# Optimization experiments

Measured on AMD Instinct MI355X. Metric: run time of the kernel, lower is better.

The kernel has to match this reference:

```python
import jax, jax.numpy as jnp
import numpy as np

E = 256   # embed_dim
L = 64    # num_landmarks
C = 256   # in_channels
N_ITER = 6


def iterative_inv(K):
    # Newton-Schulz pseudo-inverse on small [*, L, L] matrices (faithful to torch code)
    I = jnp.eye(K.shape[-1], dtype=K.dtype)
    KA = jnp.abs(K)
    V0 = KA.sum(axis=-2, keepdims=True).max(axis=-1, keepdims=True)  # [*,1,1]
    VI = KA.sum(axis=-1, keepdims=True).max(axis=-2, keepdims=True)  # [*,1,1]
    V = jnp.swapaxes(K, -1, -2) / (V0 * VI)
    for _ in range(N_ITER):
        KV = K @ V
        V = 0.25 * V @ (13.0 * I - KV @ (15.0 * I - KV @ (7.0 * I - KV)))
    return V


def setup_inputs() -> dict:
    key = jax.random.key(0)
    k0, k1, k2 = jax.random.split(key, 3)
    x = jax.random.normal(k0, (8, C, 64, 64), dtype=jnp.float32)
    # Conv2d 1x1 weights stored as [out, in]
    w_qkv = jax.random.normal(k1, (3 * E, C), dtype=jnp.float32) * 0.02
    b_qkv = jnp.zeros((3 * E,), dtype=jnp.float32)
    w_out = jax.random.normal(k2, (C, E), dtype=jnp.float32) * 0.02
    b_out = jnp.zeros((C,), dtype=jnp.float32)
    return {"x": x, "w_qkv": w_qkv, "b_qkv": b_qkv, "w_out": w_out, "b_out": b_out}


def reference(x, w_qkv, b_qkv, w_out, b_out):
    N, Cin, H, W = x.shape
    HW = H * W
    # 1x1 conv: [N, 3E, H, W]
    y = jnp.einsum('nchw,ec->nehw', x, w_qkv) + b_qkv[None, :, None, None]
    # faithful raw reshape (mixes channel/spatial like the torch code)
    qkv = y.reshape(N, HW, 3 * E)
    q, k, v = jnp.split(qkv, 3, axis=-1)                     # each [N, HW, E]
    scale = HW ** 0.5
    q_land = q.reshape(N, L, HW // L, E).mean(axis=-2) / scale  # [N, L, E]
    k_land = k.reshape(N, L, HW // L, E).mean(axis=-2) / scale  # [N, L, E]
    # three softmaxes, all over dim=-2 as in the original
    k1 = jax.nn.softmax(jnp.einsum('nie,nje->nij', q, k_land), axis=-2)       # [N, HW, L]
    k2 = jax.nn.softmax(jnp.einsum('nie,nje->nij', q_land, k_land), axis=-2)  # [N, L, L]
    k3 = jax.nn.softmax(jnp.einsum('nie,nje->nij', q_land, k), axis=-2)       # [N, L, HW]
    k2_inv = iterative_inv(k2)
    out = k1 @ (k2_inv @ (k3 @ v)) + v                        # [N, HW, E]
    out = out.reshape(N, E, H, W)                             # faithful raw reshape
    return jnp.einsum('nehw,ce->nchw', out, w_out) + b_out[None, :, None, None]
```

## Files before the change

kernel.cpp:

```cpp
#include <hip/hip_runtime.h>
#include <hip/hip_bf16.h>

typedef unsigned short u16;
typedef __attribute__((ext_vector_type(4))) float f32x4;
typedef __attribute__((ext_vector_type(8))) short short8;

#define NB   8
#define CIN  256
#define EDIM 256
#define M3   768
#define HWN  4096
#define LND  64
#define NS2  72

__device__ __forceinline__ float bf2f(u16 u){ return __uint_as_float(((unsigned)u)<<16); }
__device__ __forceinline__ u16 f2bf(float f){ __hip_bfloat16 h = __float2bfloat16(f); return *reinterpret_cast<u16*>(&h); }
__device__ __forceinline__ void bf2x2(unsigned u, float &lo, float &hi){
  lo = __uint_as_float(u<<16);
  hi = __uint_as_float(u & 0xffff0000u);
}

typedef __attribute__((address_space(1))) unsigned as1_uint;
typedef __attribute__((address_space(3))) unsigned as3_uint;
__device__ __forceinline__ void gl16(const void* g, void* l){
  __builtin_amdgcn_global_load_lds((const as1_uint*)g, (as3_uint*)l, 16, 0, 0);
}

__global__ __launch_bounds__(256) void k_prep(const float* __restrict__ x, u16* __restrict__ Xt,
                                              const float* __restrict__ wq, const float* __restrict__ wo,
                                              u16* __restrict__ Wqb, u16* __restrict__ Wob){
  const int bi = blockIdx.x;
  const int tid = threadIdx.x;
  if(bi >= 2048){
    int ti = (bi-2048)*256 + tid;
    const float* src; u16* dst;
    if(ti < 1536){ src = wq + (size_t)ti*128;        dst = Wqb + (size_t)ti*128; }
    else         { src = wo + (size_t)(ti-1536)*128; dst = Wob + (size_t)(ti-1536)*128; }
    #pragma unroll
    for(int t=0;t<128;t+=8){
      float4 v0 = *(const float4*)(src+t);
      float4 v1 = *(const float4*)(src+t+4);
      ushort4 o0, o1;
      o0.x=f2bf(v0.x); o0.y=f2bf(v0.y); o0.z=f2bf(v0.z); o0.w=f2bf(v0.w);
      o1.x=f2bf(v1.x); o1.y=f2bf(v1.y); o1.z=f2bf(v1.z); o1.w=f2bf(v1.w);
      *(ushort4*)(dst+t)   = o0;
      *(ushort4*)(dst+t+4) = o1;
    }
    return;
  }
  __shared__ float Ts[64*65];
  const int n = bi>>8, rem = bi&255, ct = rem>>6, pt = rem&63;
  const int c0 = ct*64, p0 = pt*64;
  {
    int cc = tid>>2, pj = (tid&3)*16;
    const float* xp = x + (size_t)n*CIN*HWN + (size_t)(c0+cc)*HWN + p0 + pj;
    #pragma unroll
    for(int j=0;j<16;j++) Ts[cc*65 + pj + j] = xp[j];
  }
  __syncthreads();
  {
    int pp = tid>>2, ej = (tid&3)*16;
    u16* op = Xt + ((size_t)n*HWN + p0 + pp)*CIN + c0 + ej;
    ushort4 o[4];
    #pragma unroll
    for(int j=0;j<16;j++) ((u16*)o)[j] = f2bf(Ts[(ej+j)*65 + pp]);
    *(ushort4*)(op+0)  = o[0];
    *(ushort4*)(op+4)  = o[1];
    *(ushort4*)(op+8)  = o[2];
    *(ushort4*)(op+12) = o[3];
  }
}

__global__ __launch_bounds__(256) void k_qkv(const u16* __restrict__ Wb, const u16* __restrict__ Xt,
                                             const float* __restrict__ bias, u16* __restrict__ Y){
  __shared__ __align__(16) u16 As[128*64];
  __shared__ __align__(16) u16 Bs[128*64];
  const int bi = blockIdx.x;
  const int n = bi&7, rem = bi>>3;
  const int ch0 = (rem%6)*128, p0 = (rem/6)*128;
  const int tid = threadIdx.x, lane = tid&63;
  const int c = tid&15, qq = (tid>>4)&3, w4 = tid>>6;
  const int wr0 = (w4&1)*64, wc0 = (w4>>1)*64;
  const u16* xb = Xt + ((size_t)n*HWN + p0)*CIN;
  const u16* wb = Wb + (size_t)ch0*CIN;
  f32x4 acc[4][4];
  #pragma unroll
  for(int mt=0;mt<4;mt++)
    #pragma unroll
    for(int nt=0;nt<4;nt++){ acc[mt][nt][0]=0.f; acc[mt][nt][1]=0.f; acc[mt][nt][2]=0.f; acc[mt][nt][3]=0.f; }
  const int srow  = w4*8 + (lane>>3);
  const int dslot = lane&7;
  const int sgo   = (dslot ^ (lane>>3))*8;
  const int rdswz = (c&7);
  for(int ph=0; ph<4; ph++){
    #pragma unroll
    for(int j=0;j<4;j++){
      int r = j*32 + srow;
      gl16(wb + (size_t)r*CIN + ph*64 + sgo, &As[r*64 + dslot*8]);
    }
    #pragma unroll
    for(int j=0;j<4;j++){
      int r = j*32 + srow;
      gl16(xb + (size_t)r*CIN + ph*64 + sgo, &Bs[r*64 + dslot*8]);
    }
    __syncthreads();
    #pragma unroll
    for(int kt=0;kt<2;kt++){
      short8 af[4], bff[4];
      const int rslot = ((kt*4+qq)^rdswz)*8;
      #pragma unroll
      for(int mt=0;mt<4;mt++) af[mt]  = *(const short8*)&As[(wr0+mt*16+c)*64 + rslot];
      #pragma unroll
      for(int nt=0;nt<4;nt++) bff[nt] = *(const short8*)&Bs[(wc0+nt*16+c)*64 + rslot];
      #pragma unroll
      for(int mt=0;mt<4;mt++)
        #pragma unroll
        for(int nt=0;nt<4;nt++)
          acc[mt][nt] = __builtin_amdgcn_mfma_f32_16x16x32_bf16(af[mt], bff[nt], acc[mt][nt], 0, 0, 0);
    }
    __syncthreads();
  }
  u16* Yb = Y + (size_t)n*M3*HWN;
  #pragma unroll
  for(int mt=0;mt<4;mt++){
    int chb = ch0 + wr0 + mt*16 + 4*qq;
    float b0 = bias[chb], b1 = bias[chb+1], b2 = bias[chb+2], b3 = bias[chb+3];
    #pragma unroll
    for(int nt=0;nt<4;nt++){
      int p = p0 + wc0 + nt*16 + c;
      u16* yp = Yb + (size_t)chb*HWN + p;
      yp[0]             = f2bf(acc[mt][nt][0]+b0);
      yp[HWN]           = f2bf(acc[mt][nt][1]+b1);
      yp[2*(size_t)HWN] = f2bf(acc[mt][nt][2]+b2);
      yp[3*(size_t)HWN] = f2bf(acc[mt][nt][3]+b3);
    }
  }
}

__global__ void k_land(const u16* __restrict__ Y, float* __restrict__ qland, float* __restrict__ kland){
  const int l = blockIdx.x, n = blockIdx.y, e = threadIdx.x;
  const u16* base = Y + (size_t)n*M3*HWN;
  float qs=0.f, ks=0.f;
  #pragma unroll 8
  for(int m=0;m<64;m++){
    size_t off = (size_t)(l*64+m)*M3;
    qs += bf2f(base[off+e]);
    ks += bf2f(base[off+256+e]);
  }
  qland[((size_t)n*LND+l)*EDIM+e] = qs*(1.f/4096.f);
  kland[((size_t)n*LND+l)*EDIM+e] = ks*(1.f/4096.f);
}

__device__ __forceinline__ void ns_mm2(const u16* L, int sL, const u16* Rt, int sR,
                                       int wv, int q, int c, f32x4 r4[4]){
  short8 a0 = *(const short8*)(L + (size_t)(16*wv + c)*sL + 8*q);
  short8 a1 = *(const short8*)(L + (size_t)(16*wv + c)*sL + 32 + 8*q);
  #pragma unroll
  for(int tc=0;tc<4;tc++){
    f32x4 acc = {0.f,0.f,0.f,0.f};
    short8 b0 = *(const short8*)(Rt + (size_t)(16*tc + c)*sR + 8*q);
    short8 b1 = *(const short8*)(Rt + (size_t)(16*tc + c)*sR + 32 + 8*q);
    acc = __builtin_amdgcn_mfma_f32_16x16x32_bf16(a0, b0, acc, 0, 0, 0);
    acc = __builtin_amdgcn_mfma_f32_16x16x32_bf16(a1, b1, acc, 0, 0, 0);
    r4[tc] = acc;
  }
}

#define TTS 64
__device__ void ns_body(int n, char* smem, const float* __restrict__ qland,
                        const float* __restrict__ kland, float* __restrict__ KinvT){
  u16* Kb  = (u16*)(smem + 0);
  u16* Vb  = (u16*)(smem + 9216);
  u16* Vt  = (u16*)(smem + 18432);
  u16* KVb = (u16*)(smem + 27648);
  u16* KVt = (u16*)(smem + 36864);
  u16* Tt  = (u16*)(smem + 46080);
  float* sS   = (float*)(smem + 27648);
  float* sred = (float*)(smem + 44544);
  const int tid = threadIdx.x;
  const int wv = tid>>6, q = (tid>>4)&3, c = tid&15;
  const float* qb = qland + (size_t)n*LND*EDIM;
  const float* kb = kland + (size_t)n*LND*EDIM;
  f32x4 acc[4];
  #pragma unroll
  for(int t=0;t<4;t++){ acc[t][0]=0.f; acc[t][1]=0.f; acc[t][2]=0.f; acc[t][3]=0.f; }
  for(int e0=0;e0<EDIM;e0+=64){
    __syncthreads();
    {
      int row = tid>>2, c0 = (tid&3)*16;
      const float* qp = qb + (size_t)row*EDIM + e0 + c0;
      const float* kp = kb + (size_t)row*EDIM + e0 + c0;
      u16* qd = &KVb[row*NS2 + c0];
      u16* kd = &KVt[row*NS2 + c0];
      #pragma unroll
      for(int j=0;j<16;j+=4){
        float4 qv = *(const float4*)(qp+j);
        float4 kv = *(const float4*)(kp+j);
        ushort4 qo, ko;
        qo.x=f2bf(qv.x); qo.y=f2bf(qv.y); qo.z=f2bf(qv.z); qo.w=f2bf(qv.w);
        ko.x=f2bf(kv.x); ko.y=f2bf(kv.y); ko.z=f2bf(kv.z); ko.w=f2bf(kv.w);
        *(ushort4*)(qd+j) = qo;
        *(ushort4*)(kd+j) = ko;
      }
    }
    __syncthreads();
    {
      short8 a0 = *(const short8*)&KVb[(16*wv+c)*NS2 + 8*q];
      short8 a1 = *(const short8*)&KVb[(16*wv+c)*NS2 + 32 + 8*q];
      #pragma unroll
      for(int tc=0;tc<4;tc++){
        short8 b0 = *(const short8*)&KVt[(16*tc+c)*NS2 + 8*q];
        short8 b1 = *(const short8*)&KVt[(16*tc+c)*NS2 + 32 + 8*q];
        acc[tc] = __builtin_amdgcn_mfma_f32_16x16x32_bf16(a0, b0, acc[tc], 0, 0, 0);
        acc[tc] = __builtin_amdgcn_mfma_f32_16x16x32_bf16(a1, b1, acc[tc], 0, 0, 0);
      }
    }
  }
  __syncthreads();
  #pragma unroll
  for(int tc=0;tc<4;tc++){
    int col = 16*tc + c, row0 = 16*wv + 4*q;
    sS[(row0+0)*66+col] = acc[tc][0];
    sS[(row0+1)*66+col] = acc[tc][1];
    sS[(row0+2)*66+col] = acc[tc][2];
    sS[(row0+3)*66+col] = acc[tc][3];
  }
  __syncthreads();
  if(tid < 64){
    int j = tid;
    float m = -1e30f;
    for(int i=0;i<64;i++) m = fmaxf(m, sS[i*66+j]);
    float ssum = 0.f;
    for(int i=0;i<64;i++) ssum += __expf(sS[i*66+j]-m);
    float inv = 1.f/ssum, cs = 0.f;
    for(int i=0;i<64;i++){
      float kv = __expf(sS[i*66+j]-m)*inv;
      cs += fabsf(kv);
      Kb[i*NS2+j] = f2bf(kv);
    }
    sred[j] = cs;
  }
  __syncthreads();
  if(tid < 64){
    int i = tid; float rs = 0.f;
    for(int j=0;j<64;j++) rs += fabsf(bf2f(Kb[i*NS2+j]));
    sred[64+i] = rs;
  }
  __syncthreads();
  if(tid == 0){
    float v0=-1e30f, vi=-1e30f;
    for(int t=0;t<64;t++){ v0 = fmaxf(v0, sred[t]); vi = fmaxf(vi, sred[64+t]); }
    sred[128] = 1.f/(v0*vi);
  }
  __syncthreads();
  {
    float sc = sred[128];
    int i = tid>>2, j16 = (tid&3)*16;
    #pragma unroll
    for(int jj=0;jj<16;jj++){
      int j = j16+jj;
      u16 bvv = f2bf(bf2f(Kb[j*NS2+i])*sc);
      Vb[i*NS2+j] = bvv;
      Vt[j*NS2+i] = bvv;
    }
  }
  __syncthreads();
  f32x4 r4[4];
  for(int it=0; it<6; it++){
    ns_mm2(Kb, NS2, Vt, NS2, wv, q, c, r4);
    #pragma unroll
    for(int tc=0;tc<4;tc++){
      int col = 16*tc + c, row0 = 16*wv + 4*q;
      ushort4 pk;
      pk.x = f2bf(r4[tc][0]); pk.y = f2bf(r4[tc][1]); pk.z = f2bf(r4[tc][2]); pk.w = f2bf(r4[tc][3]);
      KVb[(row0+0)*NS2+col] = pk.x; KVb[(row0+1)*NS2+col] = pk.y;
      KVb[(row0+2)*NS2+col] = pk.z; KVb[(row0+3)*NS2+col] = pk.w;
      *(ushort4*)&KVt[(size_t)col*NS2 + row0] = pk;
    }
    __syncthreads();
    ns_mm2(KVb, NS2, KVt, NS2, wv, q, c, r4);
    #pragma unroll
    for(int tc=0;tc<4;tc++){
      int col = 16*tc+c, row0 = 16*wv+4*q;
      ushort4 pk;
      #pragma unroll
      for(int r=0;r<4;r++){
        float kvv = bf2f(KVb[(row0+r)*NS2+col]);
        ((u16*)&pk)[r] = f2bf(7.f*kvv - r4[tc][r]);
      }
      *(ushort4*)&Tt[(size_t)col*TTS + row0] = pk;
    }
    __syncthreads();
    ns_mm2(KVb, NS2, Tt, TTS, wv, q, c, r4);
    __syncthreads();
    #pragma unroll
    for(int tc=0;tc<4;tc++){
      int col = 16*tc+c, row0 = 16*wv+4*q;
      ushort4 pk;
      #pragma unroll
      for(int r=0;r<4;r++){
        float kvv = bf2f(KVb[(row0+r)*NS2+col]);
        ((u16*)&pk)[r] = f2bf(15.f*kvv - r4[tc][r]);
      }
      *(ushort4*)&Tt[(size_t)col*TTS + row0] = pk;
    }
    __syncthreads();
    ns_mm2(Vb, NS2, Tt, TTS, wv, q, c, r4);
    __syncthreads();
    #pragma unroll
    for(int tc=0;tc<4;tc++){
      int col = 16*tc+c, row0 = 16*wv+4*q;
      float nv[4]; ushort4 pk;
      #pragma unroll
      for(int r=0;r<4;r++){
        float vv = bf2f(Vb[(row0+r)*NS2+col]);
        nv[r] = 0.25f*(13.f*vv - r4[tc][r]);
        u16 bb = f2bf(nv[r]);
        Vb[(row0+r)*NS2+col] = bb;
        ((u16*)&pk)[r] = bb;
      }
      *(ushort4*)&Vt[(size_t)col*NS2 + row0] = pk;
      if(it==5){
        *(float4*)&KinvT[(size_t)n*4096 + (size_t)col*64 + row0] = make_float4(nv[0],nv[1],nv[2],nv[3]);
      }
    }
    __syncthreads();
  }
}

#define LGS 264
__global__ __launch_bounds__(256) void k_landgemm(const u16* __restrict__ Y, const float* __restrict__ qland,
                                                  const float* __restrict__ kland, float* __restrict__ Z1,
                                                  float* __restrict__ Z3, float* __restrict__ KinvT){
  __shared__ __align__(16) char usm[54272];
  const int z = blockIdx.y;
  if(blockIdx.x == 64){
    if((z&1)==0) ns_body(z>>1, usm, qland, kland, KinvT);
    return;
  }
  u16* As = (u16*)usm;
  u16* BsU = (u16*)(usm + 33792);
  const int n = z>>1, which = z&1;
  const int b0 = blockIdx.x*64;
  const float* land = (which ? qland : kland) + (size_t)n*LND*EDIM;
  const int boff = which ? 256 : 0;
  float* out = (which ? Z3 : Z1) + (size_t)n*LND*HWN;
  const u16* Yb = Y + (size_t)n*M3*HWN + boff;
  const int tid = threadIdx.x, lane = tid&63;
  const int c = tid&15, qq = (tid>>4)&3, wv = tid>>6;
  {
    int r = tid>>2, c0 = (tid&3)*64;
    const float* lp = land + (size_t)r*EDIM + c0;
    u16* dp = &As[r*LGS + c0];
    #pragma unroll
    for(int j=0;j<64;j+=4){
      float4 v = *(const float4*)(lp+j);
      ushort4 o; o.x=f2bf(v.x); o.y=f2bf(v.y); o.z=f2bf(v.z); o.w=f2bf(v.w);
      *(ushort4*)(dp+j) = o;
    }
  }
  const int srow  = wv*8 + (lane>>3);
  const int dslot = lane&7;
  const int sgo   = (dslot ^ (lane>>3))*8;
  const int rdswz = (c&7);
  f32x4 acc[4];
  #pragma unroll
  for(int nt=0;nt<4;nt++){ acc[nt][0]=0.f; acc[nt][1]=0.f; acc[nt][2]=0.f; acc[nt][3]=0.f; }
  #pragma unroll
  for(int j=0;j<2;j++){
    int r = j*32 + srow;
    gl16(Yb + (size_t)(b0+r)*M3 + sgo, BsU + r*64 + dslot*8);
  }
  __syncthreads();
  for(int ph=0; ph<4; ph++){
    const int cur = ph&1;
    if(ph<3){
      #pragma unroll
      for(int j=0;j<2;j++){
        int r = j*32 + srow;
        gl16(Yb + (size_t)(b0+r)*M3 + (ph+1)*64 + sgo, BsU + (cur^1)*4096 + r*64 + dslot*8);
      }
    }
    #pragma unroll
    for(int kt=0;kt<2;kt++){
      short8 af = *(const short8*)&As[(16*wv + c)*LGS + ph*64 + kt*32 + qq*8];
      const int rslot = ((kt*4+qq)^rdswz)*8;
      #pragma unroll
      for(int nt=0;nt<4;nt++){
        short8 bff = *(const short8*)&BsU[cur*4096 + (nt*16+c)*64 + rslot];
        acc[nt] = __builtin_amdgcn_mfma_f32_16x16x32_bf16(af, bff, acc[nt], 0, 0, 0);
      }
    }
    __syncthreads();
  }
  const int m0 = 16*wv + 4*qq;
  #pragma unroll
  for(int nt=0;nt<4;nt++){
    int col = b0 + nt*16 + c;
    out[(size_t)(m0+0)*HWN + col] = acc[nt][0];
    out[(size_t)(m0+1)*HWN + col] = acc[nt][1];
    out[(size_t)(m0+2)*HWN + col] = acc[nt][2];
    out[(size_t)(m0+3)*HWN + col] = acc[nt][3];
  }
}

__device__ void soft1_body(int b, char* smem, float* __restrict__ Z1){
  const int n = b>>6, j = b&63, tid = threadIdx.x;
  float* redm = (float*)smem;
  float* reds = redm + 4;
  float* base = Z1 + ((size_t)n*LND + j)*HWN;
  float v[16];
  float m = -1e30f;
  #pragma unroll
  for(int r=0;r<16;r++){ v[r] = base[r*256 + tid]; m = fmaxf(m, v[r]); }
  #pragma unroll
  for(int o=32;o;o>>=1) m = fmaxf(m, __shfl_xor(m, o));
  const int wid = tid>>6;
  if((tid&63)==0) redm[wid] = m;
  __syncthreads();
  m = fmaxf(fmaxf(redm[0],redm[1]), fmaxf(redm[2],redm[3]));
  float s = 0.f;
  #pragma unroll
  for(int r=0;r<16;r++){ v[r] = __expf(v[r]-m); s += v[r]; }
  #pragma unroll
  for(int o=32;o;o>>=1) s += __shfl_xor(s, o);
  if((tid&63)==0) reds[wid] = s;
  __syncthreads();
  s = reds[0]+reds[1]+reds[2]+reds[3];
  float inv = 1.f/s;
  #pragma unroll
  for(int r=0;r<16;r++) base[r*256 + tid] = v[r]*inv;
}

__global__ __launch_bounds__(256) void k_pv(const float* __restrict__ Z3, const u16* __restrict__ Y,
                                            float* __restrict__ part, float* __restrict__ Z1){
  __shared__ __align__(16) char smem[50688];
  const int bi = blockIdx.x;
  if(bi >= 512){ soft1_body(bi-512, smem, Z1); return; }
  float* Sf   = (float*)smem;
  float* sinv = (float*)(smem + 33792);
  u16*   Asb  = (u16*)(smem + 34304);
  u16*   Vt   = (u16*)smem;
  const int kc = bi&31, n = (bi>>5)&7, eh = bi>>8;
  const int jb = kc*128, eb = eh*128;
  const int tid = threadIdx.x, lane = tid&63;
  const int c = tid&15, qq = (tid>>4)&3, wv = tid>>6;
  const u16* Yb = Y + (size_t)n*M3*HWN;
  const float* z3b = Z3 + (size_t)n*LND*HWN;
  {
    int ibase = (tid>>5)*8, j4 = (tid&31)*4;
    #pragma unroll
    for(int r=0;r<8;r++){
      int i = ibase + r;
      *(float4*)&Sf[i*132 + j4] = *(const float4*)&z3b[(size_t)i*HWN + jb + j4];
    }
  }
  __syncthreads();
  if(tid < 128){
    int j = tid;
    float m = -1e30f;
    for(int i=0;i<64;i++) m = fmaxf(m, Sf[i*132 + j]);
    float s = 0.f;
    for(int i=0;i<64;i++){ float e = __expf(Sf[i*132 + j] - m); Sf[i*132 + j] = e; s += e; }
    sinv[j] = 1.f/s;
  }
  __syncthreads();
  {
    int i = tid>>2, j0q = (tid&3)*32;
    const int iswz = (i&7);
    #pragma unroll
    for(int t=0;t<32;t+=4){
      int jg = j0q + t;
      int phb = jg>>6, jl = jg&63;
      ushort4 o;
      o.x = f2bf(Sf[i*132 + jg+0]*sinv[jg+0]);
      o.y = f2bf(Sf[i*132 + jg+1]*sinv[jg+1]);
      o.z = f2bf(Sf[i*132 + jg+2]*sinv[jg+2]);
      o.w = f2bf(Sf[i*132 + jg+3]*sinv[jg+3]);
      *(ushort4*)&Asb[phb*4096 + i*64 + ((jl>>3)^iswz)*8 + (jl&7)] = o;
    }
  }
  __syncthreads();
  const int rdswz = (c&7);
  f32x4 acc[4][2];
  #pragma unroll
  for(int mt=0;mt<4;mt++)
    #pragma unroll
    for(int nt=0;nt<2;nt++){ acc[mt][nt][0]=0.f; acc[mt][nt][1]=0.f; acc[mt][nt][2]=0.f; acc[mt][nt][3]=0.f; }
  for(int ph=0; ph<2; ph++){
    #pragma unroll
    for(int rep=0; rep<4; rep++){
      int jl = (tid>>4) + 16*rep;
      int ec = (tid&15)*8;
      uint4 U = *(const uint4*)&Yb[(size_t)(jb+ph*64+jl)*M3 + 512 + eb + ec];
      const u16* uv = (const u16*)&U;
      #pragma unroll
      for(int k=0;k<8;k++){
        int e = ec+k;
        int slot = ((jl>>3) ^ (e&7) ^ ((e>>3)&7)) & 7;
        Vt[e*64 + slot*8 + (jl&7)] = uv[k];
      }
    }
    __syncthreads();
    #pragma unroll
    for(int kt=0;kt<2;kt++){
      const int rslotA = ((kt*4+qq)^rdswz)*8;
      short8 af[4];
      #pragma unroll
      for(int mt=0;mt<4;mt++) af[mt] = *(const short8*)&Asb[ph*4096 + (mt*16+c)*64 + rslotA];
      #pragma unroll
      for(int nt=0;nt<2;nt++){
        int e = wv*32 + nt*16 + c;
        int slotB = ((kt*4+qq) ^ (e&7) ^ ((e>>3)&7)) & 7;
        short8 bf_ = *(const short8*)&Vt[e*64 + slotB*8];
        #pragma unroll
        for(int mt=0;mt<4;mt++)
          acc[mt][nt] = __builtin_amdgcn_mfma_f32_16x16x32_bf16(af[mt], bf_, acc[mt][nt], 0, 0, 0);
      }
    }
    __syncthreads();
  }
  float* pb = part + ((size_t)n*32 + kc)*LND*EDIM + eb;
  #pragma unroll
  for(int mt=0;mt<4;mt++){
    int row0 = mt*16 + 4*qq;
    #pragma unroll
    for(int nt=0;nt<2;nt++){
      int e = wv*32 + nt*16 + c;
      pb[(size_t)(row0+0)*EDIM + e] = acc[mt][nt][0];
      pb[(size_t)(row0+1)*EDIM + e] = acc[mt][nt][1];
      pb[(size_t)(row0+2)*EDIM + e] = acc[mt][nt][2];
      pb[(size_t)(row0+3)*EDIM + e] = acc[mt][nt][3];
    }
  }
}

__global__ __launch_bounds__(256) void k_c2(const float* __restrict__ KinvT, const float* __restrict__ part,
                                            u16* __restrict__ C2T){
  const int eb = blockIdx.x*64, n = blockIdx.y, tid = threadIdx.x;
  __shared__ float KT[64][68];
  __shared__ float Bs2[64][68];
  __shared__ u16 Ct[64*72];
  {
    int l = tid>>2, o16 = (tid&3)*16;
    const float* kp = KinvT + (size_t)n*4096 + l*64 + o16;
    #pragma unroll
    for(int t=0;t<16;t+=4) *(float4*)&KT[l][o16+t] = *(const float4*)(kp+t);
    const float* pp = part + (size_t)n*32*16384 + (size_t)l*256 + eb + o16;
    float4 s0 = {0,0,0,0}, s1 = {0,0,0,0}, s2 = {0,0,0,0}, s3 = {0,0,0,0};
    for(int kc=0;kc<32;kc++){
      const float* b = pp + (size_t)kc*16384;
      float4 v0 = *(const float4*)(b);
      float4 v1 = *(const float4*)(b+4);
      float4 v2 = *(const float4*)(b+8);
      float4 v3 = *(const float4*)(b+12);
      s0.x+=v0.x; s0.y+=v0.y; s0.z+=v0.z; s0.w+=v0.w;
      s1.x+=v1.x; s1.y+=v1.y; s1.z+=v1.z; s1.w+=v1.w;
      s2.x+=v2.x; s2.y+=v2.y; s2.z+=v2.z; s2.w+=v2.w;
      s3.x+=v3.x; s3.y+=v3.y; s3.z+=v3.z; s3.w+=v3.w;
    }
    *(float4*)&Bs2[l][o16+0]  = s0;
    *(float4*)&Bs2[l][o16+4]  = s1;
    *(float4*)&Bs2[l][o16+8]  = s2;
    *(float4*)&Bs2[l][o16+12] = s3;
  }
  __syncthreads();
  const int j0 = (tid>>4)*4, u0 = (tid&15)*4;
  float acc[4][4] = {};
  #pragma unroll 8
  for(int l=0;l<64;l++){
    f32x4 a = *(f32x4*)&KT[l][j0];
    f32x4 b = *(f32x4*)&Bs2[l][u0];
    #pragma unroll
    for(int s=0;s<4;s++)
      #pragma unroll
      for(int u=0;u<4;u++) acc[s][u] += a[s]*b[u];
  }
  #pragma unroll
  for(int s=0;s<4;s++)
    #pragma unroll
    for(int u=0;u<4;u++)
      Ct[(u0+u)*72 + j0+s] = f2bf(acc[s][u]);
  __syncthreads();
  {
    int e = tid>>2, j16 = (tid&3)*16;
    u16* op = C2T + ((size_t)n*256 + eb + e)*64 + j16;
    #pragma unroll
    for(int t=0;t<16;t+=4)
      *(ushort4*)(op+t) = *(const ushort4*)&Ct[e*72 + j16 + t];
  }
}

__global__ __launch_bounds__(256) void k_out(const float* __restrict__ Z1, const u16* __restrict__ C2T,
                                             const u16* __restrict__ Y, u16* __restrict__ OM){
  __shared__ __align__(16) u16 Cs[256*64];
  __shared__ __align__(16) u16 Zt[64*72];
  const int ib = blockIdx.x*64, n = blockIdx.y;
  const int tid = threadIdx.x, lane = tid&63;
  const int c = tid&15, qq = (tid>>4)&3, wv = tid>>6;
  const int srow  = wv*8 + (lane>>3);
  const int dslot = lane&7;
  const int sgo   = (dslot ^ (lane>>3))*8;
  const int rdswz = (c&7);
  const u16* cb = C2T + (size_t)n*256*64;
  #pragma unroll
  for(int j=0;j<8;j++){
    int r = j*32 + srow;
    gl16(cb + (size_t)r*64 + sgo, &Cs[r*64 + dslot*8]);
  }
  {
    int j = tid>>2, i16 = (tid&3)*16;
    const float* zp = Z1 + ((size_t)n*LND + j)*HWN + ib + i16;
    #pragma unroll
    for(int t=0;t<16;t+=4){
      float4 v = *(const float4*)(zp+t);
      Zt[(i16+t+0)*72 + j] = f2bf(v.x);
      Zt[(i16+t+1)*72 + j] = f2bf(v.y);
      Zt[(i16+t+2)*72 + j] = f2bf(v.z);
      Zt[(i16+t+3)*72 + j] = f2bf(v.w);
    }
  }
  __syncthreads();
  f32x4 acc[4][4];
  #pragma unroll
  for(int mt=0;mt<4;mt++)
    #pragma unroll
    for(int nt=0;nt<4;nt++){ acc[mt][nt][0]=0.f; acc[mt][nt][1]=0.f; acc[mt][nt][2]=0.f; acc[mt][nt][3]=0.f; }
  #pragma unroll
  for(int kt=0;kt<2;kt++){
    const int rslot = ((kt*4+qq)^rdswz)*8;
    short8 af[4], bf_[4];
    #pragma unroll
    for(int mt=0;mt<4;mt++) af[mt] = *(const short8*)&Cs[(wv*64+mt*16+c)*64 + rslot];
    #pragma unroll
    for(int nt=0;nt<4;nt++) bf_[nt] = *(const short8*)&Zt[(nt*16+c)*72 + kt*32 + qq*8];
    #pragma unroll
    for(int mt=0;mt<4;mt++)
      #pragma unroll
      for(int nt=0;nt<4;nt++)
        acc[mt][nt] = __builtin_amdgcn_mfma_f32_16x16x32_bf16(af[mt], bf_[nt], acc[mt][nt], 0, 0, 0);
  }
  const u16* Yb = Y + (size_t)n*M3*HWN;
  u16* ob = OM + (size_t)n*HWN*EDIM;
  #pragma unroll
  for(int mt=0;mt<4;mt++){
    int e = wv*64 + mt*16 + 4*qq;
    #pragma unroll
    for(int nt=0;nt<4;nt++){
      int i = ib + nt*16 + c;
      ushort4 V4 = *(const ushort4*)(Yb + (size_t)i*M3 + 512 + e);
      ushort4 o;
      o.x = f2bf(acc[mt][nt][0] + bf2f(V4.x));
      o.y = f2bf(acc[mt][nt][1] + bf2f(V4.y));
      o.z = f2bf(acc[mt][nt][2] + bf2f(V4.z));
      o.w = f2bf(acc[mt][nt][3] + bf2f(V4.w));
      *(ushort4*)(ob + (size_t)i*EDIM + e) = o;
    }
  }
}

__global__ __launch_bounds__(256) void k_proj(const u16* __restrict__ Wb, const u16* __restrict__ OM,
                                              const float* __restrict__ bias, float* __restrict__ out){
  __shared__ __align__(16) u16 As[128*64];
  __shared__ __align__(16) u16 Bt[128*64];
  const int bi = blockIdx.x;
  const int n = bi&7, rem = bi>>3;
  const int ch0 = (rem&1)*128, p0 = (rem>>1)*128;
  const int tid = threadIdx.x, lane = tid&63;
  const int c = tid&15, qq = (tid>>4)&3, w4 = tid>>6;
  const int wr0 = (w4&1)*64, wc0 = (w4>>1)*64;
  const u16* omb = OM + (size_t)n*HWN*EDIM;
  const u16* wb = Wb + (size_t)ch0*EDIM;
  f32x4 acc[4][4];
  #pragma unroll
  for(int mt=0;mt<4;mt++)
    #pragma unroll
    for(int nt=0;nt<4;nt++){ acc[mt][nt][0]=0.f; acc[mt][nt][1]=0.f; acc[mt][nt][2]=0.f; acc[mt][nt][3]=0.f; }
  const int srow  = w4*8 + (lane>>3);
  const int dslot = lane&7;
  const int sgo   = (dslot ^ (lane>>3))*8;
  const int rdswz = (c&7);
  for(int ph=0; ph<4; ph++){
    #pragma unroll
    for(int j=0;j<4;j++){
      int r = j*32 + srow;
      gl16(wb + (size_t)r*EDIM + ph*64 + sgo, &As[r*64 + dslot*8]);
    }
    #pragma unroll
    for(int rep=0; rep<4; rep++){
      int ee = (tid>>4) + 16*rep;
      int pc = (tid&15)*8;
      uint4 U = *(const uint4*)&omb[(size_t)(ph*64+ee)*HWN + p0 + pc];
      const u16* uv = (const u16*)&U;
      #pragma unroll
      for(int k=0;k<8;k++){
        int p = pc+k;
        int slot = ((ee>>3) ^ (p&7) ^ ((p>>3)&7)) & 7;
        Bt[p*64 + slot*8 + (ee&7)] = uv[k];
      }
    }
    __syncthreads();
    #pragma unroll
    for(int kt=0;kt<2;kt++){
      const int rslot = ((kt*4+qq)^rdswz)*8;
      short8 af[4], bff[4];
      #pragma unroll
      for(int mt=0;mt<4;mt++) af[mt] = *(const short8*)&As[(wr0+mt*16+c)*64 + rslot];
      #pragma unroll
      for(int nt=0;nt<4;nt++){
        int p = wc0 + nt*16 + c;
        int slotB = ((kt*4+qq) ^ (p&7) ^ ((p>>3)&7)) & 7;
        bff[nt] = *(const short8*)&Bt[p*64 + slotB*8];
      }
      #pragma unroll
      for(int mt=0;mt<4;mt++)
        #pragma unroll
        for(int nt=0;nt<4;nt++)
          acc[mt][nt] = __builtin_amdgcn_mfma_f32_16x16x32_bf16(af[mt], bff[nt], acc[mt][nt], 0, 0, 0);
    }
    __syncthreads();
  }
  float* ob = out + (size_t)n*EDIM*HWN;
  #pragma unroll
  for(int mt=0;mt<4;mt++){
    int chb = ch0 + wr0 + mt*16 + 4*qq;
    float b0 = bias[chb], b1 = bias[chb+1], b2 = bias[chb+2], b3 = bias[chb+3];
    #pragma unroll
    for(int nt=0;nt<4;nt++){
      int p = p0 + wc0 + nt*16 + c;
      float* yp = ob + (size_t)chb*HWN + p;
      yp[0]             = acc[mt][nt][0]+b0;
      yp[HWN]           = acc[mt][nt][1]+b1;
      yp[2*(size_t)HWN] = acc[mt][nt][2]+b2;
      yp[3*(size_t)HWN] = acc[mt][nt][3]+b3;
    }
  }
}

extern "C" void kernel_launch(void* const* d_in, const int* in_sizes, int n_in,
                              void* d_out, int out_size, void* d_ws, size_t ws_size,
                              hipStream_t stream){
  (void)out_size; (void)ws_size;
  const float* x     = (const float*)d_in[0];
  const float* w_qkv = (const float*)d_in[1];
  const float* b_qkv = (const float*)d_in[2];
  const float* w_out = (const float*)d_in[3];
  const float* b_out = (const float*)d_in[4];
  for(int i=0;i<n_in;i++){
    switch(in_sizes[i]){
      case 8388608: x     = (const float*)d_in[i]; break;
      case 196608:  w_qkv = (const float*)d_in[i]; break;
      case 768:     b_qkv = (const float*)d_in[i]; break;
      case 65536:   w_out = (const float*)d_in[i]; break;
      case 256:     b_out = (const float*)d_in[i]; break;
      default: break;
    }
  }
  float* out = (float*)d_out;
  char* ws = (char*)d_ws;

  u16*   Y     = (u16*)(ws + 0);
  float* qland = (float*)(ws + 50331648);
  float* kland = (float*)(ws + 50855936);
  float* Z1    = (float*)(ws + 51380224);
  float* Z3    = (float*)(ws + 59768832);
  float* KinvT = (float*)(ws + 68157440);
  float* part  = (float*)(ws + 68288512);
  u16*   Xt    = (u16*)(ws + 68288512);
  u16*   C2T   = (u16*)(ws + 85065728);
  u16*   OM    = (u16*)(ws + 86114304);
  u16*   Wqb   = (u16*)(ws + 59768832);
  u16*   Wob   = (u16*)(ws + 102891520);

  k_prep    <<<dim3(2056),   256, 0, stream>>>(x, Xt, w_qkv, w_out, Wqb, Wob);
  k_qkv     <<<dim3(1536),   256, 0, stream>>>(Wqb, Xt, b_qkv, Y);
  k_land    <<<dim3(64,8),   256, 0, stream>>>(Y, qland, kland);
  k_landgemm<<<dim3(65,16),  256, 0, stream>>>(Y, qland, kland, Z1, Z3, KinvT);
  k_pv      <<<dim3(1024),   256, 0, stream>>>(Z3, Y, part, Z1);
  k_c2      <<<dim3(4,8),    256, 0, stream>>>(KinvT, part, C2T);
  k_out     <<<dim3(64,8),   256, 0, stream>>>(Z1, C2T, Y, OM);
  k_proj    <<<dim3(512),    256, 0, stream>>>(Wob, OM, b_out, out);
}
```

Before: 202.5 us.

## Run Newton-Schulz inverse in a single wavefront to drop block barriers

The landmark-score GEMM, softmax and Newton-Schulz iterations now run in one 64-lane wavefront that computes the full 64x64 tiles itself. This removes all __syncthreads barriers and shared-memory reductions, replacing them with wave shuffles. The cost is 4x more MFMA work and larger register tiles per wave, since the other three waves idle. The inverse block runs alongside the GEMM blocks, so its latency may or may not be on the critical path.

```diff
diff --git a/kernel.cpp b/kernel.cpp
--- a/kernel.cpp
+++ b/kernel.cpp
@@ -151,83 +151,77 @@
   kland[((size_t)n*LND+l)*EDIM+e] = ks*(1.f/4096.f);
 }
 
-__device__ __forceinline__ void ns_mm2(const u16* L, int sL, const u16* Rt, int sR,
-                                       int wv, int q, int c, f32x4 r4[4]){
-  short8 a0 = *(const short8*)(L + (size_t)(16*wv + c)*sL + 8*q);
-  short8 a1 = *(const short8*)(L + (size_t)(16*wv + c)*sL + 32 + 8*q);
+__device__ __forceinline__ void ns_mm_w(const u16* L, int sL, const u16* Rt, int sR,
+                                        int q, int c, f32x4 out[4][4]){
+  short8 bfr[4][2];
   #pragma unroll
   for(int tc=0;tc<4;tc++){
-    f32x4 acc = {0.f,0.f,0.f,0.f};
-    short8 b0 = *(const short8*)(Rt + (size_t)(16*tc + c)*sR + 8*q);
-    short8 b1 = *(const short8*)(Rt + (size_t)(16*tc + c)*sR + 32 + 8*q);
-    acc = __builtin_amdgcn_mfma_f32_16x16x32_bf16(a0, b0, acc, 0, 0, 0);
-    acc = __builtin_amdgcn_mfma_f32_16x16x32_bf16(a1, b1, acc, 0, 0, 0);
-    r4[tc] = acc;
+    bfr[tc][0] = *(const short8*)(Rt + (size_t)(16*tc + c)*sR + 8*q);
+    bfr[tc][1] = *(const short8*)(Rt + (size_t)(16*tc + c)*sR + 32 + 8*q);
+  }
+  #pragma unroll
+  for(int mt=0;mt<4;mt++){
+    short8 a0 = *(const short8*)(L + (size_t)(16*mt + c)*sL + 8*q);
+    short8 a1 = *(const short8*)(L + (size_t)(16*mt + c)*sL + 32 + 8*q);
+    #pragma unroll
+    for(int tc=0;tc<4;tc++){
+      f32x4 v = out[mt][tc];
+      v = __builtin_amdgcn_mfma_f32_16x16x32_bf16(a0, bfr[tc][0], v, 0, 0, 0);
+      v = __builtin_amdgcn_mfma_f32_16x16x32_bf16(a1, bfr[tc][1], v, 0, 0, 0);
+      out[mt][tc] = v;
+    }
   }
 }
 
 #define TTS 64
-__device__ void ns_body(int n, char* smem, const float* __restrict__ qland,
-                        const float* __restrict__ kland, float* __restrict__ KinvT){
+__device__ void ns_body_w(int n, char* smem, const float* __restrict__ qland,
+                          const float* __restrict__ kland, float* __restrict__ KinvT){
   u16* Kb  = (u16*)(smem + 0);
   u16* Vb  = (u16*)(smem + 9216);
   u16* Vt  = (u16*)(smem + 18432);
   u16* KVb = (u16*)(smem + 27648);
   u16* KVt = (u16*)(smem + 36864);
   u16* Tt  = (u16*)(smem + 46080);
-  float* sS   = (float*)(smem + 27648);
-  float* sred = (float*)(smem + 44544);
-  const int tid = threadIdx.x;
-  const int wv = tid>>6, q = (tid>>4)&3, c = tid&15;
+  float* sS = (float*)(smem + 27648);
+  const int lane = threadIdx.x;
+  const int q = (lane>>4)&3, c = lane&15;
   const float* qb = qland + (size_t)n*LND*EDIM;
   const float* kb = kland + (size_t)n*LND*EDIM;
-  f32x4 acc[4];
-  #pragma unroll
-  for(int t=0;t<4;t++){ acc[t][0]=0.f; acc[t][1]=0.f; acc[t][2]=0.f; acc[t][3]=0.f; }
+  f32x4 acc[4][4];
+  #pragma unroll
+  for(int mt=0;mt<4;mt++)
+    #pragma unroll
+    for(int tc=0;tc<4;tc++){ acc[mt][tc][0]=0.f; acc[mt][tc][1]=0.f; acc[mt][tc][2]=0.f; acc[mt][tc][3]=0.f; }
   for(int e0=0;e0<EDIM;e0+=64){
-    __syncthreads();
-    {
-      int row = tid>>2, c0 = (tid&3)*16;
-      const float* qp = qb + (size_t)row*EDIM + e0 + c0;
-      const float* kp = kb + (size_t)row*EDIM + e0 + c0;
-      u16* qd = &KVb[row*NS2 + c0];
-      u16* kd = &KVt[row*NS2 + c0];
-      #pragma unroll
-      for(int j=0;j<16;j+=4){
-        float4 qv = *(const float4*)(qp+j);
-        float4 kv = *(const float4*)(kp+j);
-        ushort4 qo, ko;
-        qo.x=f2bf(qv.x); qo.y=f2bf(qv.y); qo.z=f2bf(qv.z); qo.w=f2bf(qv.w);
-        ko.x=f2bf(kv.x); ko.y=f2bf(kv.y); ko.z=f2bf(kv.z); ko.w=f2bf(kv.w);
-        *(ushort4*)(qd+j) = qo;
-        *(ushort4*)(kd+j) = ko;
-      }
-    }
-    __syncthreads();
-    {
-      short8 a0 = *(const short8*)&KVb[(16*wv+c)*NS2 + 8*q];
-      short8 a1 = *(const short8*)&KVb[(16*wv+c)*NS2 + 32 + 8*q];
-      #pragma unroll
-      for(int tc=0;tc<4;tc++){
-        short8 b0 = *(const short8*)&KVt[(16*tc+c)*NS2 + 8*q];
-        short8 b1 = *(const short8*)&KVt[(16*tc+c)*NS2 + 32 + 8*q];
-        acc[tc] = __builtin_amdgcn_mfma_f32_16x16x32_bf16(a0, b0, acc[tc], 0, 0, 0);
-        acc[tc] = __builtin_amdgcn_mfma_f32_16x16x32_bf16(a1, b1, acc[tc], 0, 0, 0);
-      }
-    }
-  }
-  __syncthreads();
-  #pragma unroll
-  for(int tc=0;tc<4;tc++){
-    int col = 16*tc + c, row0 = 16*wv + 4*q;
-    sS[(row0+0)*66+col] = acc[tc][0];
-    sS[(row0+1)*66+col] = acc[tc][1];
-    sS[(row0+2)*66+col] = acc[tc][2];
-    sS[(row0+3)*66+col] = acc[tc][3];
-  }
-  __syncthreads();
-  if(tid < 64){
-    int j = tid;
+    const float* qp = qb + (size_t)lane*EDIM + e0;
+    const float* kp = kb + (size_t)lane*EDIM + e0;
+    u16* qd = &KVb[lane*NS2];
+    u16* kd = &KVt[lane*NS2];
+    #pragma unroll
+    for(int j=0;j<64;j+=4){
+      float4 qv = *(const float4*)(qp+j);
+      float4 kv = *(const float4*)(kp+j);
+      ushort4 qo, ko;
+      qo.x=f2bf(qv.x); qo.y=f2bf(qv.y); qo.z=f2bf(qv.z); qo.w=f2bf(qv.w);
+      ko.x=f2bf(kv.x); ko.y=f2bf(kv.y); ko.z=f2bf(kv.z); ko.w=f2bf(kv.w);
+      *(ushort4*)(qd+j) = qo;
+      *(ushort4*)(kd+j) = ko;
+    }
+    ns_mm_w(KVb, NS2, KVt, NS2, q, c, acc);
+  }
+  #pragma unroll
+  for(int mt=0;mt<4;mt++)
+    #pragma unroll
+    for(int tc=0;tc<4;tc++){
+      int col = 16*tc + c, row0 = 16*mt + 4*q;
+      sS[(row0+0)*66+col] = acc[mt][tc][0];
+      sS[(row0+1)*66+col] = acc[mt][tc][1];
+      sS[(row0+2)*66+col] = acc[mt][tc][2];
+      sS[(row0+3)*66+col] = acc[mt][tc][3];
+    }
+  float sc;
+  {
+    int j = lane;
     float m = -1e30f;
     for(int i=0;i<64;i++) m = fmaxf(m, sS[i*66+j]);
     float ssum = 0.f;
@@ -238,93 +232,100 @@
       cs += fabsf(kv);
       Kb[i*NS2+j] = f2bf(kv);
     }
-    sred[j] = cs;
-  }
-  __syncthreads();
-  if(tid < 64){
-    int i = tid; float rs = 0.f;
-    for(int j=0;j<64;j++) rs += fabsf(bf2f(Kb[i*NS2+j]));
-    sred[64+i] = rs;
-  }
-  __syncthreads();
-  if(tid == 0){
-    float v0=-1e30f, vi=-1e30f;
-    for(int t=0;t<64;t++){ v0 = fmaxf(v0, sred[t]); vi = fmaxf(vi, sred[64+t]); }
-    sred[128] = 1.f/(v0*vi);
-  }
-  __syncthreads();
-  {
-    float sc = sred[128];
-    int i = tid>>2, j16 = (tid&3)*16;
-    #pragma unroll
-    for(int jj=0;jj<16;jj++){
-      int j = j16+jj;
-      u16 bvv = f2bf(bf2f(Kb[j*NS2+i])*sc);
-      Vb[i*NS2+j] = bvv;
-      Vt[j*NS2+i] = bvv;
-    }
-  }
-  __syncthreads();
-  f32x4 r4[4];
+    float v0 = cs;
+    #pragma unroll
+    for(int o=32;o;o>>=1) v0 = fmaxf(v0, __shfl_xor(v0, o));
+    float rs = 0.f;
+    for(int jj=0;jj<64;jj++) rs += fabsf(bf2f(Kb[lane*NS2+jj]));
+    float vi = rs;
+    #pragma unroll
+    for(int o=32;o;o>>=1) vi = fmaxf(vi, __shfl_xor(vi, o));
+    sc = 1.f/(v0*vi);
+  }
+  for(int jj=0;jj<64;jj++){
+    u16 bvv = f2bf(bf2f(Kb[jj*NS2+lane])*sc);
+    Vb[lane*NS2+jj] = bvv;
+    Vt[jj*NS2+lane] = bvv;
+  }
+  f32x4 r[4][4];
   for(int it=0; it<6; it++){
-    ns_mm2(Kb, NS2, Vt, NS2, wv, q, c, r4);
-    #pragma unroll
-    for(int tc=0;tc<4;tc++){
-      int col = 16*tc + c, row0 = 16*wv + 4*q;
-      ushort4 pk;
-      pk.x = f2bf(r4[tc][0]); pk.y = f2bf(r4[tc][1]); pk.z = f2bf(r4[tc][2]); pk.w = f2bf(r4[tc][3]);
-      KVb[(row0+0)*NS2+col] = pk.x; KVb[(row0+1)*NS2+col] = pk.y;
-      KVb[(row0+2)*NS2+col] = pk.z; KVb[(row0+3)*NS2+col] = pk.w;
-      *(ushort4*)&KVt[(size_t)col*NS2 + row0] = pk;
-    }
-    __syncthreads();
-    ns_mm2(KVb, NS2, KVt, NS2, wv, q, c, r4);
-    #pragma unroll
-    for(int tc=0;tc<4;tc++){
-      int col = 16*tc+c, row0 = 16*wv+4*q;
-      ushort4 pk;
-      #pragma unroll
-      for(int r=0;r<4;r++){
-        float kvv = bf2f(KVb[(row0+r)*NS2+col]);
-        ((u16*)&pk)[r] = f2bf(7.f*kvv - r4[tc][r]);
-      }
-      *(ushort4*)&Tt[(size_t)col*TTS + row0] = pk;
-    }
-    __syncthreads();
-    ns_mm2(KVb, NS2, Tt, TTS, wv, q, c, r4);
-    __syncthreads();
-    #pragma unroll
-    for(int tc=0;tc<4;tc++){
-      int col = 16*tc+c, row0 = 16*wv+4*q;
-      ushort4 pk;
-      #pragma unroll
-      for(int r=0;r<4;r++){
-        float kvv = bf2f(KVb[(row0+r)*NS2+col]);
-        ((u16*)&pk)[r] = f2bf(15.f*kvv - r4[tc][r]);
-      }
-      *(ushort4*)&Tt[(size_t)col*TTS + row0] = pk;
-    }
-    __syncthreads();
-    ns_mm2(Vb, NS2, Tt, TTS, wv, q, c, r4);
-    __syncthreads();
-    #pragma unroll
-    for(int tc=0;tc<4;tc++){
-      int col = 16*tc+c, row0 = 16*wv+4*q;
-      float nv[4]; ushort4 pk;
-      #pragma unroll
-      for(int r=0;r<4;r++){
-        float vv = bf2f(Vb[(row0+r)*NS2+col]);
-        nv[r] = 0.25f*(13.f*vv - r4[tc][r]);
-        u16 bb = f2bf(nv[r]);
-        Vb[(row0+r)*NS2+col] = bb;
-        ((u16*)&pk)[r] = bb;
-      }
-      *(ushort4*)&Vt[(size_t)col*NS2 + row0] = pk;
-      if(it==5){
-        *(float4*)&KinvT[(size_t)n*4096 + (size_t)col*64 + row0] = make_float4(nv[0],nv[1],nv[2],nv[3]);
-      }
-    }
-    __syncthreads();
+    #pragma unroll
+    for(int mt=0;mt<4;mt++)
+      #pragma unroll
+      for(int tc=0;tc<4;tc++){ r[mt][tc][0]=0.f; r[mt][tc][1]=0.f; r[mt][tc][2]=0.f; r[mt][tc][3]=0.f; }
+    ns_mm_w(Kb, NS2, Vt, NS2, q, c, r);
+    #pragma unroll
+    for(int mt=0;mt<4;mt++)
+      #pragma unroll
+      for(int tc=0;tc<4;tc++){
+        int col = 16*tc + c, row0 = 16*mt + 4*q;
+        ushort4 pk;
+        pk.x = f2bf(r[mt][tc][0]); pk.y = f2bf(r[mt][tc][1]);
+        pk.z = f2bf(r[mt][tc][2]); pk.w = f2bf(r[mt][tc][3]);
+        KVb[(row0+0)*NS2+col] = pk.x; KVb[(row0+1)*NS2+col] = pk.y;
+        KVb[(row0+2)*NS2+col] = pk.z; KVb[(row0+3)*NS2+col] = pk.w;
+        *(ushort4*)&KVt[(size_t)col*NS2 + row0] = pk;
+      }
+    #pragma unroll
+    for(int mt=0;mt<4;mt++)
+      #pragma unroll
+      for(int tc=0;tc<4;tc++){ r[mt][tc][0]=0.f; r[mt][tc][1]=0.f; r[mt][tc][2]=0.f; r[mt][tc][3]=0.f; }
+    ns_mm_w(KVb, NS2, KVt, NS2, q, c, r);
+    #pragma unroll
+    for(int mt=0;mt<4;mt++)
+      #pragma unroll
+      for(int tc=0;tc<4;tc++){
+        int col = 16*tc+c, row0 = 16*mt+4*q;
+        ushort4 pk;
+        #pragma unroll
+        for(int rr=0;rr<4;rr++){
+          float kvv = bf2f(KVb[(row0+rr)*NS2+col]);
+          ((u16*)&pk)[rr] = f2bf(7.f*kvv - r[mt][tc][rr]);
+        }
+        *(ushort4*)&Tt[(size_t)col*TTS + row0] = pk;
+      }
+    #pragma unroll
+    for(int mt=0;mt<4;mt++)
+      #pragma unroll
+      for(int tc=0;tc<4;tc++){ r[mt][tc][0]=0.f; r[mt][tc][1]=0.f; r[mt][tc][2]=0.f; r[mt][tc][3]=0.f; }
+    ns_mm_w(KVb, NS2, Tt, TTS, q, c, r);
+    #pragma unroll
+    for(int mt=0;mt<4;mt++)
+      #pragma unroll
+      for(int tc=0;tc<4;tc++){
+        int col = 16*tc+c, row0 = 16*mt+4*q;
+        ushort4 pk;
+        #pragma unroll
+        for(int rr=0;rr<4;rr++){
+          float kvv = bf2f(KVb[(row0+rr)*NS2+col]);
+          ((u16*)&pk)[rr] = f2bf(15.f*kvv - r[mt][tc][rr]);
+        }
+        *(ushort4*)&KVt[(size_t)col*NS2 + row0] = pk;
+      }
+    #pragma unroll
+    for(int mt=0;mt<4;mt++)
+      #pragma unroll
+      for(int tc=0;tc<4;tc++){ r[mt][tc][0]=0.f; r[mt][tc][1]=0.f; r[mt][tc][2]=0.f; r[mt][tc][3]=0.f; }
+    ns_mm_w(Vb, NS2, KVt, NS2, q, c, r);
+    #pragma unroll
+    for(int mt=0;mt<4;mt++)
+      #pragma unroll
+      for(int tc=0;tc<4;tc++){
+        int col = 16*tc+c, row0 = 16*mt+4*q;
+        float nv[4]; ushort4 pk;
+        #pragma unroll
+        for(int rr=0;rr<4;rr++){
+          float vv = bf2f(Vb[(row0+rr)*NS2+col]);
+          nv[rr] = 0.25f*(13.f*vv - r[mt][tc][rr]);
+          u16 bb = f2bf(nv[rr]);
+          Vb[(row0+rr)*NS2+col] = bb;
+          ((u16*)&pk)[rr] = bb;
+        }
+        *(ushort4*)&Vt[(size_t)col*NS2 + row0] = pk;
+        if(it==5){
+          *(float4*)&KinvT[(size_t)n*4096 + (size_t)col*64 + row0] = make_float4(nv[0],nv[1],nv[2],nv[3]);
+        }
+      }
   }
 }
 
@@ -335,7 +336,7 @@
   __shared__ __align__(16) char usm[54272];
   const int z = blockIdx.y;
   if(blockIdx.x == 64){
-    if((z&1)==0) ns_body(z>>1, usm, qland, kland, KinvT);
+    if((z&1)==0 && threadIdx.x < 64) ns_body_w(z>>1, usm, qland, kland, KinvT);
     return;
   }
   u16* As = (u16*)usm;
```

New measurement: 231.2 us. +14.2%, slower.
